# Optimization experiments

Hardware: AMD Instinct MI355X
Metric: run time of the kernel (lower is better)

The kernel has to match this reference:

```python
import jax, jax.numpy as jnp
import numpy as np

EMBED_DIM = 1024
CONTEXT_LEN = 2048
NUM_HEADS = 16
HEAD_DIM = EMBED_DIM // NUM_HEADS
BATCH = 2
SEQ = 2048


def setup_inputs() -> dict:
    key = jax.random.key(0)
    ks = jax.random.split(key, 6)
    s = 1.0 / np.sqrt(EMBED_DIM)
    x = jax.random.normal(ks[0], (BATCH, SEQ, EMBED_DIM), dtype=jnp.float32)
    # nn.Linear weights stored as [out, in]; we keep [in, out] for x @ W
    W_q = jax.random.uniform(ks[1], (EMBED_DIM, EMBED_DIM), jnp.float32, -s, s)
    W_k = jax.random.uniform(ks[2], (EMBED_DIM, EMBED_DIM), jnp.float32, -s, s)
    W_v = jax.random.uniform(ks[3], (EMBED_DIM, EMBED_DIM), jnp.float32, -s, s)
    W_o = jax.random.uniform(ks[4], (EMBED_DIM, EMBED_DIM), jnp.float32, -s, s)
    b_o = jax.random.uniform(ks[5], (EMBED_DIM,), jnp.float32, -s, s)
    return {"x": x, "W_q": W_q, "W_k": W_k, "W_v": W_v, "W_o": W_o, "b_o": b_o}


def reference(x, W_q, W_k, W_v, W_o, b_o):
    b, s, _ = x.shape
    # project and split heads: [b, s, e] -> [b, h, s, d]
    def heads(t):
        return t.reshape(b, s, NUM_HEADS, HEAD_DIM).transpose(0, 2, 1, 3)
    q = heads(x @ W_q)
    k = heads(x @ W_k)
    v = heads(x @ W_v)
    scores = jnp.einsum("bhqd,bhkd->bhqk", q, k)  # full seq x seq scores
    causal = jnp.triu(jnp.ones((s, s), dtype=bool), k=1)
    scores = jnp.where(causal, -jnp.inf, scores)
    attn = jax.nn.softmax(scores / np.sqrt(HEAD_DIM).astype(np.float32), axis=-1)
    ctx = jnp.einsum("bhqk,bhkd->bhqd", attn, v)
    ctx = ctx.transpose(0, 2, 1, 3).reshape(b, s, EMBED_DIM)
    return ctx @ W_o + b_o
```

## Files before the change

kernel.cpp:

```cpp
#include <hip/hip_runtime.h>

#define EMBED 1024
#define SEQL  2048
#define NHEAD 16
#define HDIM  64
#define NBATCH 2
#define MROWS 4096

typedef __attribute__((ext_vector_type(4))) float  f32x4;
typedef __attribute__((ext_vector_type(8))) __bf16 bf16x8;

__device__ __forceinline__ short f2bf(float f){
  __bf16 h = (__bf16)f;
  union { __bf16 h; short s; } u; u.h = h;
  return u.s;
}

#define GLDS(gp, lp) __builtin_amdgcn_global_load_lds( \
    (const __attribute__((address_space(1))) void*)(gp), \
    (__attribute__((address_space(3))) void*)(lp), 16, 0, 0)

__global__ __launch_bounds__(256) void prep_kernel(const float* __restrict__ x,
    const float* __restrict__ W0, const float* __restrict__ W1,
    const float* __restrict__ W2, const float* __restrict__ W3,
    short* __restrict__ Xb, short* __restrict__ WtAll){
  const int z = blockIdx.z;
  if (z < 4){
    __shared__ float T[64][65];
    const int idx = blockIdx.y*32 + blockIdx.x;
    if (idx >= 256) return;
    const float* W = (z==0)?W0:(z==1)?W1:(z==2)?W2:W3;
    short* Wt = WtAll + z*(EMBED*EMBED);
    const int bx = (idx & 15)*64;
    const int by = (idx >> 4)*64;
    const int c4 = (threadIdx.x & 15)*4;
    const int tr = threadIdx.x >> 4;
    #pragma unroll
    for (int i=0;i<4;++i){
      int r = 16*i + tr;
      float4 v = *(const float4*)(W + (by + r)*EMBED + bx + c4);
      T[c4+0][r] = v.x; T[c4+1][r] = v.y; T[c4+2][r] = v.z; T[c4+3][r] = v.w;
    }
    __syncthreads();
    #pragma unroll
    for (int i=0;i<4;++i){
      int n = 16*i + tr;
      short4 o;
      o.x = f2bf(T[n][c4+0]); o.y = f2bf(T[n][c4+1]);
      o.z = f2bf(T[n][c4+2]); o.w = f2bf(T[n][c4+3]);
      *(short4*)(Wt + (bx + n)*EMBED + by + c4) = o;
    }
  } else {
    const int blk = (z-4)*1024 + blockIdx.y*32 + blockIdx.x;
    const int i = (blk*256 + threadIdx.x)*4;
    float4 v = *(const float4*)(x + i);
    short4 o; o.x=f2bf(v.x); o.y=f2bf(v.y); o.z=f2bf(v.z); o.w=f2bf(v.w);
    *(short4*)(Xb + i) = o;
  }
}

__device__ __forceinline__ void gemm_tile_128(const short* __restrict__ A,
    const short* __restrict__ Bt, short* As, short* Bs, int m0, int n0, f32x4 acc[4][4]){
  const int tid  = threadIdx.x;
  const int lane = tid & 63;
  const int wid  = tid >> 6;
  const int wrow = (wid >> 1) * 64, wcol = (wid & 1) * 64;
  const int arow = tid >> 2, acol8 = (tid & 3) * 8;
  const int l15 = lane & 15, lg = lane >> 4;

  auto STAGE = [&](int b, int k0){
    short* as = As + b*4096;
    short* bs = Bs + b*4096;
    GLDS(A  + (m0      + arow) * 1024 + k0 + acol8, as + tid*8);
    GLDS(A  + (m0 + 64 + arow) * 1024 + k0 + acol8, as + 2048 + tid*8);
    GLDS(Bt + (n0      + arow) * 1024 + k0 + acol8, bs + tid*8);
    GLDS(Bt + (n0 + 64 + arow) * 1024 + k0 + acol8, bs + 2048 + tid*8);
  };

  auto KSTEP = [&](int b){
    const short* as = As + b*4096;
    const short* bs = Bs + b*4096;
    bf16x8 a[4], bb[4];
    #pragma unroll
    for (int i=0;i<4;++i) a[i]  = *(const bf16x8*)(as + (wrow+16*i+l15)*32 + 8*lg);
    #pragma unroll
    for (int j=0;j<4;++j) bb[j] = *(const bf16x8*)(bs + (wcol+16*j+l15)*32 + 8*lg);
    #pragma unroll
    for (int i=0;i<4;++i)
      #pragma unroll
      for (int j=0;j<4;++j)
        acc[i][j] = __builtin_amdgcn_mfma_f32_16x16x32_bf16(a[i], bb[j], acc[i][j], 0,0,0);
  };

  STAGE(0, 0); STAGE(1, 32);
  __syncthreads();
  for (int p = 0; p < 16; ++p){
    const int k0 = p*64;
    if (p + 1 < 16){ STAGE((2*p+2)&3, k0+64); STAGE((2*p+3)&3, k0+96); }
    KSTEP((2*p)&3);
    KSTEP((2*p+1)&3);
    __syncthreads();
  }
}

__device__ __forceinline__ void gemm_tile_64(const short* __restrict__ A,
    const short* __restrict__ Bt, short* As, short* Bs, int m0, int n0, f32x4 acc[2][4]){
  const int tid  = threadIdx.x;
  const int lane = tid & 63;
  const int wid  = tid >> 6;
  const int wrow = (wid >> 1) * 32, wcol = (wid & 1) * 64;
  const int arow = tid >> 2, acol8 = (tid & 3) * 8;
  const int l15 = lane & 15, lg = lane >> 4;

  auto STAGE = [&](int b, int k0){
    short* as = As + b*2048;
    short* bs = Bs + b*4096;
    GLDS(A  + (m0      + arow) * 1024 + k0 + acol8, as + tid*8);
    GLDS(Bt + (n0      + arow) * 1024 + k0 + acol8, bs + tid*8);
    GLDS(Bt + (n0 + 64 + arow) * 1024 + k0 + acol8, bs + 2048 + tid*8);
  };

  auto KSTEP = [&](int b){
    const short* as = As + b*2048;
    const short* bs = Bs + b*4096;
    bf16x8 a[2], bb[4];
    #pragma unroll
    for (int i=0;i<2;++i) a[i]  = *(const bf16x8*)(as + (wrow+16*i+l15)*32 + 8*lg);
    #pragma unroll
    for (int j=0;j<4;++j) bb[j] = *(const bf16x8*)(bs + (wcol+16*j+l15)*32 + 8*lg);
    #pragma unroll
    for (int i=0;i<2;++i)
      #pragma unroll
      for (int j=0;j<4;++j)
        acc[i][j] = __builtin_amdgcn_mfma_f32_16x16x32_bf16(a[i], bb[j], acc[i][j], 0,0,0);
  };

  STAGE(0, 0); STAGE(1, 32);
  __syncthreads();
  for (int p = 0; p < 16; ++p){
    const int k0 = p*64;
    if (p + 1 < 16){ STAGE((2*p+2)&3, k0+64); STAGE((2*p+3)&3, k0+96); }
    KSTEP((2*p)&3);
    KSTEP((2*p+1)&3);
    __syncthreads();
  }
}

__global__ __launch_bounds__(256) void gemm_qkv_kernel(const short* __restrict__ Xb,
    const short* __restrict__ WtAll, short* __restrict__ Q, short* __restrict__ K,
    short* __restrict__ Vt){
  __shared__ __align__(16) short SH[32768];
  short* As = SH;
  short* Bs = SH + 16384;
  const int m0 = blockIdx.x*128, n0 = blockIdx.y*128, z = blockIdx.z;
  const short* Bt = WtAll + z*(EMBED*EMBED);
  f32x4 acc[4][4] = {};
  gemm_tile_128(Xb, Bt, As, Bs, m0, n0, acc);
  const int tid  = threadIdx.x;
  const int lane = tid & 63;
  const int wid  = tid >> 6;
  const int wrow = (wid >> 1) * 64, wcol = (wid & 1) * 64;
  const int l15 = lane & 15, lg = lane >> 4;
  const int bb = m0 >> 11, srow0 = m0 & 2047;

  if (z < 2){
    short* out = z ? K : Q;
    const float qscl = (z==0) ? (0.125f * 1.44269504f) : 1.0f;
    #pragma unroll
    for (int i=0;i<4;++i)
      #pragma unroll
      for (int j=0;j<4;++j)
        #pragma unroll
        for (int r=0;r<4;++r){
          int m = m0 + wrow + 16*i + 4*lg + r;
          int n = n0 + wcol + 16*j + l15;
          int srow = m & 2047, hh = n >> 6, d = n & 63;
          out[(((bb<<4)+hh)*SEQL + srow)*HDIM + d] = f2bf(acc[i][j][r] * qscl);
        }
  } else {
    short* T = SH;
    #pragma unroll
    for (int i=0;i<4;++i)
      #pragma unroll
      for (int j=0;j<4;++j){
        int n_loc = wcol + 16*j + l15;
        int mb    = wrow + 16*i + 4*lg;
        short4 pk;
        pk.x = f2bf(acc[i][j][0]); pk.y = f2bf(acc[i][j][1]);
        pk.z = f2bf(acc[i][j][2]); pk.w = f2bf(acc[i][j][3]);
        *(short4*)(T + n_loc*128 + (mb ^ ((n_loc & 7) << 3))) = pk;
      }
    __syncthreads();
    #pragma unroll
    for (int it=0; it<8; ++it){
      int n_loc = 16*it + (tid >> 4);
      int mch   = (tid & 15) * 8;
      int4 v = *(const int4*)(T + n_loc*128 + (mch ^ ((n_loc & 7) << 3)));
      int n_glob = n0 + n_loc;
      int hh = n_glob >> 6, d = n_glob & 63;
      *(int4*)(Vt + (((bb<<4)+hh)*HDIM + d)*SEQL + srow0 + mch) = v;
    }
  }
}

__global__ __launch_bounds__(256) void gemm_out_kernel(const short* __restrict__ Ctx,
    const short* __restrict__ WtO, const float* __restrict__ bias, float* __restrict__ out){
  __shared__ __align__(16) short As[4*2048], Bs[4*4096];
  const int m0 = blockIdx.x*64, n0 = blockIdx.y*128;
  f32x4 acc[2][4] = {};
  gemm_tile_64(Ctx, WtO, As, Bs, m0, n0, acc);
  const int lane = threadIdx.x & 63;
  const int wid  = threadIdx.x >> 6;
  const int wrow = (wid >> 1) * 32, wcol = (wid & 1) * 64;
  const int l15 = lane & 15, lg = lane >> 4;
  #pragma unroll
  for (int i=0;i<2;++i)
    #pragma unroll
    for (int j=0;j<4;++j)
      #pragma unroll
      for (int r=0;r<4;++r){
        int m = m0 + wrow + 16*i + 4*lg + r;
        int n = n0 + wcol + 16*j + l15;
        out[m*EMBED + n] = acc[i][j][r] + bias[n];
      }
}

__global__ __launch_bounds__(512, 4) void attn_kernel(const short* __restrict__ Q,
    const short* __restrict__ K, const short* __restrict__ Vt, short* __restrict__ Ctx){
  __shared__ __align__(16) char lds[81920];
  const int tid  = threadIdx.x;
  const int lane = tid & 63;
  const int wid  = tid >> 6;
  const int bid   = blockIdx.x;
  const int xcd   = bid & 7;
  const int i7    = bid >> 3;
  const int bh    = xcd + 8*(i7 & 3);
  const int cidx  = i7 >> 2;
  const int chunk = (cidx < 8) ? cidx : 23 - cidx;
  const int q0blk = chunk * 128;
  const int ntp   = chunk + 1;
  const int q0w   = q0blk + 16*wid;
  const int qlast = q0w + 15;

  const short* Qh  = Q  + bh*(SEQL*HDIM);
  const char*  KhB = (const char*)(K  + bh*(SEQL*HDIM));
  const char*  VhB = (const char*)(Vt + bh*(HDIM*SEQL));
  const int l15 = lane & 15, lg = lane >> 4;
  const int lg20 = 20 * lg;
  const int swE = (l15 & 7) << 3;
  const int swB = (l15 & 7) << 4;
  const int laneRow = lane >> 3;
  const int colSwz  = 16 * ((lane & 7) ^ laneRow);
  const int r0 = 8 * wid;

  const short* qp = Qh + (q0w + l15)*HDIM + 8*lg;
  bf16x8 bq0 = *(const bf16x8*)qp;
  bf16x8 bq1 = *(const bf16x8*)(qp + 32);

  f32x4 acc[4];
  #pragma unroll
  for (int j=0; j<4; ++j) acc[j] = (f32x4){0.f,0.f,0.f,0.f};
  float mrun = -3e30f, lrun = 0.f;

  short* pw = (short*)(lds + 65536 + wid*2048);

  auto STAGE = [&](int b, int t){
    char* kb = lds + b*16384;
    char* vb = kb + 8192;
    const int kv0 = t*64;
    GLDS(KhB + (kv0 + r0 + laneRow)*128 + colSwz, kb + r0*128);
    GLDS(VhB + (r0 + laneRow)*4096 + kv0*2 + colSwz, vb + r0*128);
  };

  auto QKHALF = [&](const char* kb, f32x4 sc[4]){
    #pragma unroll
    for (int c=0; c<4; ++c){
      const char* kr = kb + (16*c + l15)*128;
      bf16x8 k0 = *(const bf16x8*)(kr + ((16*lg) ^ swB));
      bf16x8 k1 = *(const bf16x8*)(kr + ((64 + 16*lg) ^ swB));
      f32x4 zz = (f32x4){0.f,0.f,0.f,0.f};
      zz = __builtin_amdgcn_mfma_f32_16x16x32_bf16(k0, bq0, zz, 0,0,0);
      zz = __builtin_amdgcn_mfma_f32_16x16x32_bf16(k1, bq1, zz, 0,0,0);
      sc[c] = zz;
    }
  };

  STAGE(0, 0); STAGE(1, 1);
  __syncthreads();

  for (int tp = 0; tp < ntp; ++tp){
    const int t0   = 2*tp;
    const int kv00 = t0*64;
    const int kv01 = kv00 + 64;
    if (tp + 1 < ntp){ STAGE((t0+2)&3, t0+2); STAGE((t0+3)&3, t0+3); }
    if (kv00 <= qlast){
      const char* kb0 = lds + (t0&3)*16384;
      const char* kb1 = lds + ((t0+1)&3)*16384;
      const bool  h1  = (kv01 <= qlast);
      f32x4 sc0[4], sc1[4];
      __builtin_amdgcn_s_setprio(1);
      QKHALF(kb0, sc0);
      if (h1) QKHALF(kb1, sc1);
      __builtin_amdgcn_s_setprio(0);
      if (kv00 + 63 > q0w){
        #pragma unroll
        for (int c=0; c<4; ++c)
          #pragma unroll
          for (int r=0; r<4; ++r)
            if (kv00 + 16*c + 4*lg + r > q0w + l15) sc0[c][r] = -3e30f;
      }
      if (h1 && kv01 + 63 > q0w){
        #pragma unroll
        for (int c=0; c<4; ++c)
          #pragma unroll
          for (int r=0; r<4; ++r)
            if (kv01 + 16*c + 4*lg + r > q0w + l15) sc1[c][r] = -3e30f;
      }
      float cm[4];
      #pragma unroll
      for (int c=0; c<4; ++c)
        cm[c] = fmaxf(fmaxf(sc0[c][0], sc0[c][1]), fmaxf(sc0[c][2], sc0[c][3]));
      float pm = fmaxf(fmaxf(cm[0], cm[1]), fmaxf(cm[2], cm[3]));
      if (h1){
        float dm[4];
        #pragma unroll
        for (int c=0; c<4; ++c)
          dm[c] = fmaxf(fmaxf(sc1[c][0], sc1[c][1]), fmaxf(sc1[c][2], sc1[c][3]));
        pm = fmaxf(pm, fmaxf(fmaxf(dm[0], dm[1]), fmaxf(dm[2], dm[3])));
      }
      pm = fmaxf(pm, __shfl_xor(pm, 16));
      pm = fmaxf(pm, __shfl_xor(pm, 32));
      const int resc = !__all(pm <= mrun);
      float mn = mrun, ss = 1.0f;
      if (resc){
        mn = fmaxf(mrun, pm);
        ss = __builtin_amdgcn_exp2f(mrun - mn);
        mrun = mn;
      }
      #pragma unroll
      for (int c=0; c<4; ++c)
        #pragma unroll
        for (int r=0; r<4; ++r)
          sc0[c][r] = __builtin_amdgcn_exp2f(sc0[c][r] - mn);
      float cs[4];
      #pragma unroll
      for (int c=0; c<4; ++c)
        cs[c] = (sc0[c][0] + sc0[c][1]) + (sc0[c][2] + sc0[c][3]);
      float ls = (cs[0] + cs[1]) + (cs[2] + cs[3]);
      if (h1){
        #pragma unroll
        for (int c=0; c<4; ++c)
          #pragma unroll
          for (int r=0; r<4; ++r)
            sc1[c][r] = __builtin_amdgcn_exp2f(sc1[c][r] - mn);
        float ds[4];
        #pragma unroll
        for (int c=0; c<4; ++c)
          ds[c] = (sc1[c][0] + sc1[c][1]) + (sc1[c][2] + sc1[c][3]);
        ls += (ds[0] + ds[1]) + (ds[2] + ds[3]);
      }
      ls += __shfl_xor(ls, 16);
      ls += __shfl_xor(ls, 32);
      if (resc){
        lrun = lrun*ss + ls;
        float srg[4];
        #pragma unroll
        for (int r=0; r<4; ++r) srg[r] = __shfl(ss, lg20 + r);
        #pragma unroll
        for (int j=0; j<4; ++j)
          #pragma unroll
          for (int r=0; r<4; ++r) acc[j][r] *= srg[r];
      } else {
        lrun += ls;
      }
      #pragma unroll
      for (int c=0; c<4; ++c){
        short4 pk;
        pk.x = f2bf(sc0[c][0]); pk.y = f2bf(sc0[c][1]);
        pk.z = f2bf(sc0[c][2]); pk.w = f2bf(sc0[c][3]);
        *(short4*)(pw + l15*64 + ((16*c + 4*lg) ^ swE)) = pk;
      }
      {
        bf16x8 pa0 = *(const bf16x8*)(pw + l15*64 + ((8*lg)      ^ swE));
        bf16x8 pa1 = *(const bf16x8*)(pw + l15*64 + ((32 + 8*lg) ^ swE));
        const char* vb = kb0 + 8192;
        __builtin_amdgcn_s_setprio(1);
        #pragma unroll
        for (int j=0; j<4; ++j){
          const char* vrp = vb + (16*j + l15)*128;
          bf16x8 v0 = *(const bf16x8*)(vrp + ((16*lg) ^ swB));
          bf16x8 v1 = *(const bf16x8*)(vrp + ((64 + 16*lg) ^ swB));
          acc[j] = __builtin_amdgcn_mfma_f32_16x16x32_bf16(pa0, v0, acc[j], 0,0,0);
          acc[j] = __builtin_amdgcn_mfma_f32_16x16x32_bf16(pa1, v1, acc[j], 0,0,0);
        }
        __builtin_amdgcn_s_setprio(0);
      }
      if (h1){
        #pragma unroll
        for (int c=0; c<4; ++c){
          short4 pk;
          pk.x = f2bf(sc1[c][0]); pk.y = f2bf(sc1[c][1]);
          pk.z = f2bf(sc1[c][2]); pk.w = f2bf(sc1[c][3]);
          *(short4*)(pw + l15*64 + ((16*c + 4*lg) ^ swE)) = pk;
        }
        bf16x8 pa0 = *(const bf16x8*)(pw + l15*64 + ((8*lg)      ^ swE));
        bf16x8 pa1 = *(const bf16x8*)(pw + l15*64 + ((32 + 8*lg) ^ swE));
        const char* vb = kb1 + 8192;
        __builtin_amdgcn_s_setprio(1);
        #pragma unroll
        for (int j=0; j<4; ++j){
          const char* vrp = vb + (16*j + l15)*128;
          bf16x8 v0 = *(const bf16x8*)(vrp + ((16*lg) ^ swB));
          bf16x8 v1 = *(const bf16x8*)(vrp + ((64 + 16*lg) ^ swB));
          acc[j] = __builtin_amdgcn_mfma_f32_16x16x32_bf16(pa0, v0, acc[j], 0,0,0);
          acc[j] = __builtin_amdgcn_mfma_f32_16x16x32_bf16(pa1, v1, acc[j], 0,0,0);
        }
        __builtin_amdgcn_s_setprio(0);
      }
    }
    __syncthreads();
  }

  const int bb = bh >> 4, hh = bh & 15;
  float lr[4];
  #pragma unroll
  for (int r=0; r<4; ++r) lr[r] = __builtin_amdgcn_rcpf(__shfl(lrun, lg20 + r));
  #pragma unroll
  for (int j=0; j<4; ++j)
    #pragma unroll
    for (int r=0; r<4; ++r){
      int qg = q0w + 4*lg + r;
      Ctx[(bb*SEQL + qg)*EMBED + hh*HDIM + 16*j + l15] = f2bf(acc[j][r] * lr[r]);
    }
}

extern "C" void kernel_launch(void* const* d_in, const int* in_sizes, int n_in,
                              void* d_out, int out_size, void* d_ws, size_t ws_size,
                              hipStream_t stream){
  const float* x  = (const float*)d_in[0];
  const float* Wq = (const float*)d_in[1];
  const float* Wk = (const float*)d_in[2];
  const float* Wv = (const float*)d_in[3];
  const float* Wo = (const float*)d_in[4];
  const float* bo = (const float*)d_in[5];
  float* out = (float*)d_out;

  char* ws = (char*)d_ws;
  const size_t MB = 1u << 20;
  short* Xb  = (short*)(ws +  0*MB);
  short* Wt  = (short*)(ws +  8*MB);
  short* Q   = (short*)(ws + 16*MB);
  short* Kk  = (short*)(ws + 24*MB);
  short* Vt  = (short*)(ws + 32*MB);
  short* Ctx = (short*)(ws + 40*MB);

  prep_kernel<<<dim3(32,32,8), 256, 0, stream>>>(x, Wq, Wk, Wv, Wo, Xb, Wt);
  gemm_qkv_kernel<<<dim3(32,8,3), 256, 0, stream>>>(Xb, Wt, Q, Kk, Vt);
  attn_kernel<<<512, 512, 0, stream>>>(Q, Kk, Vt, Ctx);
  gemm_out_kernel<<<dim3(64,8), 256, 0, stream>>>(Ctx, Wt + 3*(EMBED*EMBED), bo, out);
}
```

Measured before the change: 101.6 us.

## Split attention KV range across wave halves with two query groups per wave

Each wave now handles 32 query rows (two 16-row groups) rather than 16, and the 8 waves are split into two halves that each process half of the causal KV tiles for the same rows. At the end, partial softmax states (max, sum, accumulator) from the second half are exchanged through LDS and merged flash-decoding style before writing the context. This is meant to balance causal work across waves and reuse each K/V fragment load for two query groups, at the cost of more registers, an extra LDS merge and a final barrier.

```diff
diff --git a/kernel.cpp b/kernel.cpp
--- a/kernel.cpp
+++ b/kernel.cpp
@@ -231,6 +231,8 @@
   const int tid  = threadIdx.x;
   const int lane = tid & 63;
   const int wid  = tid >> 6;
+  const int wrg  = wid & 3;
+  const int khalf= wid >> 2;
   const int bid   = blockIdx.x;
   const int xcd   = bid & 7;
   const int i7    = bid >> 3;
@@ -238,9 +240,12 @@
   const int cidx  = i7 >> 2;
   const int chunk = (cidx < 8) ? cidx : 23 - cidx;
   const int q0blk = chunk * 128;
-  const int ntp   = chunk + 1;
-  const int q0w   = q0blk + 16*wid;
-  const int qlast = q0w + 15;
+  const int ntblk = 2*chunk + 2;
+  const int q0w   = q0blk + 32*wrg;
+  const int nt_w  = ((q0w + 31) >> 6) + 1;
+  const int h0    = (nt_w + 1) >> 1;
+  const int tbeg  = khalf ? h0 : 0;
+  const int tend  = khalf ? nt_w : h0;
 
   const short* Qh  = Q  + bh*(SEQL*HDIM);
   const char*  KhB = (const char*)(K  + bh*(SEQL*HDIM));
@@ -253,14 +258,22 @@
   const int colSwz  = 16 * ((lane & 7) ^ laneRow);
   const int r0 = 8 * wid;
 
-  const short* qp = Qh + (q0w + l15)*HDIM + 8*lg;
-  bf16x8 bq0 = *(const bf16x8*)qp;
-  bf16x8 bq1 = *(const bf16x8*)(qp + 32);
-
-  f32x4 acc[4];
+  bf16x8 bq[2][2];
   #pragma unroll
-  for (int j=0; j<4; ++j) acc[j] = (f32x4){0.f,0.f,0.f,0.f};
-  float mrun = -3e30f, lrun = 0.f;
+  for (int g=0; g<2; ++g){
+    const short* qp = Qh + (q0w + 16*g + l15)*HDIM + 8*lg;
+    bq[g][0] = *(const bf16x8*)qp;
+    bq[g][1] = *(const bf16x8*)(qp + 32);
+  }
+
+  f32x4 acc[2][4];
+  float mrun[2], lrun[2];
+  #pragma unroll
+  for (int g=0; g<2; ++g){
+    mrun[g] = -3e30f; lrun[g] = 0.f;
+    #pragma unroll
+    for (int j=0; j<4; ++j) acc[g][j] = (f32x4){0.f,0.f,0.f,0.f};
+  }
 
   short* pw = (short*)(lds + 65536 + wid*2048);
 
@@ -272,166 +285,160 @@
     GLDS(VhB + (r0 + laneRow)*4096 + kv0*2 + colSwz, vb + r0*128);
   };
 
-  auto QKHALF = [&](const char* kb, f32x4 sc[4]){
+  auto TILE = [&](int tt){
+    const char* kb = lds + (tt&3)*16384;
+    const char* vb = kb + 8192;
+    const int kv0 = tt*64;
+    f32x4 sc[4][2];
+    __builtin_amdgcn_s_setprio(1);
     #pragma unroll
     for (int c=0; c<4; ++c){
       const char* kr = kb + (16*c + l15)*128;
       bf16x8 k0 = *(const bf16x8*)(kr + ((16*lg) ^ swB));
       bf16x8 k1 = *(const bf16x8*)(kr + ((64 + 16*lg) ^ swB));
-      f32x4 zz = (f32x4){0.f,0.f,0.f,0.f};
-      zz = __builtin_amdgcn_mfma_f32_16x16x32_bf16(k0, bq0, zz, 0,0,0);
-      zz = __builtin_amdgcn_mfma_f32_16x16x32_bf16(k1, bq1, zz, 0,0,0);
-      sc[c] = zz;
-    }
-  };
-
-  STAGE(0, 0); STAGE(1, 1);
-  __syncthreads();
-
-  for (int tp = 0; tp < ntp; ++tp){
-    const int t0   = 2*tp;
-    const int kv00 = t0*64;
-    const int kv01 = kv00 + 64;
-    if (tp + 1 < ntp){ STAGE((t0+2)&3, t0+2); STAGE((t0+3)&3, t0+3); }
-    if (kv00 <= qlast){
-      const char* kb0 = lds + (t0&3)*16384;
-      const char* kb1 = lds + ((t0+1)&3)*16384;
-      const bool  h1  = (kv01 <= qlast);
-      f32x4 sc0[4], sc1[4];
-      __builtin_amdgcn_s_setprio(1);
-      QKHALF(kb0, sc0);
-      if (h1) QKHALF(kb1, sc1);
-      __builtin_amdgcn_s_setprio(0);
-      if (kv00 + 63 > q0w){
-        #pragma unroll
-        for (int c=0; c<4; ++c)
+      #pragma unroll
+      for (int g=0; g<2; ++g){
+        f32x4 zz = (f32x4){0.f,0.f,0.f,0.f};
+        zz = __builtin_amdgcn_mfma_f32_16x16x32_bf16(k0, bq[g][0], zz, 0,0,0);
+        zz = __builtin_amdgcn_mfma_f32_16x16x32_bf16(k1, bq[g][1], zz, 0,0,0);
+        sc[c][g] = zz;
+      }
+    }
+    __builtin_amdgcn_s_setprio(0);
+    if (kv0 + 63 > q0w){
+      #pragma unroll
+      for (int c=0; c<4; ++c)
+        #pragma unroll
+        for (int g=0; g<2; ++g)
           #pragma unroll
           for (int r=0; r<4; ++r)
-            if (kv00 + 16*c + 4*lg + r > q0w + l15) sc0[c][r] = -3e30f;
-      }
-      if (h1 && kv01 + 63 > q0w){
-        #pragma unroll
-        for (int c=0; c<4; ++c)
-          #pragma unroll
-          for (int r=0; r<4; ++r)
-            if (kv01 + 16*c + 4*lg + r > q0w + l15) sc1[c][r] = -3e30f;
-      }
+            if (kv0 + 16*c + 4*lg + r > q0w + 16*g + l15) sc[c][g][r] = -3e30f;
+    }
+    #pragma unroll
+    for (int g=0; g<2; ++g){
       float cm[4];
       #pragma unroll
       for (int c=0; c<4; ++c)
-        cm[c] = fmaxf(fmaxf(sc0[c][0], sc0[c][1]), fmaxf(sc0[c][2], sc0[c][3]));
+        cm[c] = fmaxf(fmaxf(sc[c][g][0], sc[c][g][1]), fmaxf(sc[c][g][2], sc[c][g][3]));
       float pm = fmaxf(fmaxf(cm[0], cm[1]), fmaxf(cm[2], cm[3]));
-      if (h1){
-        float dm[4];
-        #pragma unroll
-        for (int c=0; c<4; ++c)
-          dm[c] = fmaxf(fmaxf(sc1[c][0], sc1[c][1]), fmaxf(sc1[c][2], sc1[c][3]));
-        pm = fmaxf(pm, fmaxf(fmaxf(dm[0], dm[1]), fmaxf(dm[2], dm[3])));
-      }
       pm = fmaxf(pm, __shfl_xor(pm, 16));
       pm = fmaxf(pm, __shfl_xor(pm, 32));
-      const int resc = !__all(pm <= mrun);
-      float mn = mrun, ss = 1.0f;
+      const int resc = !__all(pm <= mrun[g]);
+      float mn = mrun[g], ss = 1.0f;
       if (resc){
-        mn = fmaxf(mrun, pm);
-        ss = __builtin_amdgcn_exp2f(mrun - mn);
-        mrun = mn;
+        mn = fmaxf(mrun[g], pm);
+        ss = __builtin_amdgcn_exp2f(mrun[g] - mn);
+        mrun[g] = mn;
       }
       #pragma unroll
       for (int c=0; c<4; ++c)
         #pragma unroll
         for (int r=0; r<4; ++r)
-          sc0[c][r] = __builtin_amdgcn_exp2f(sc0[c][r] - mn);
+          sc[c][g][r] = __builtin_amdgcn_exp2f(sc[c][g][r] - mn);
       float cs[4];
       #pragma unroll
       for (int c=0; c<4; ++c)
-        cs[c] = (sc0[c][0] + sc0[c][1]) + (sc0[c][2] + sc0[c][3]);
+        cs[c] = (sc[c][g][0] + sc[c][g][1]) + (sc[c][g][2] + sc[c][g][3]);
       float ls = (cs[0] + cs[1]) + (cs[2] + cs[3]);
-      if (h1){
-        #pragma unroll
-        for (int c=0; c<4; ++c)
-          #pragma unroll
-          for (int r=0; r<4; ++r)
-            sc1[c][r] = __builtin_amdgcn_exp2f(sc1[c][r] - mn);
-        float ds[4];
-        #pragma unroll
-        for (int c=0; c<4; ++c)
-          ds[c] = (sc1[c][0] + sc1[c][1]) + (sc1[c][2] + sc1[c][3]);
-        ls += (ds[0] + ds[1]) + (ds[2] + ds[3]);
-      }
       ls += __shfl_xor(ls, 16);
       ls += __shfl_xor(ls, 32);
       if (resc){
-        lrun = lrun*ss + ls;
+        lrun[g] = lrun[g]*ss + ls;
         float srg[4];
         #pragma unroll
         for (int r=0; r<4; ++r) srg[r] = __shfl(ss, lg20 + r);
         #pragma unroll
         for (int j=0; j<4; ++j)
           #pragma unroll
-          for (int r=0; r<4; ++r) acc[j][r] *= srg[r];
+          for (int r=0; r<4; ++r) acc[g][j][r] *= srg[r];
       } else {
-        lrun += ls;
-      }
+        lrun[g] += ls;
+      }
+    }
+    bf16x8 pa[2][2];
+    #pragma unroll
+    for (int g=0; g<2; ++g){
       #pragma unroll
       for (int c=0; c<4; ++c){
         short4 pk;
-        pk.x = f2bf(sc0[c][0]); pk.y = f2bf(sc0[c][1]);
-        pk.z = f2bf(sc0[c][2]); pk.w = f2bf(sc0[c][3]);
+        pk.x = f2bf(sc[c][g][0]); pk.y = f2bf(sc[c][g][1]);
+        pk.z = f2bf(sc[c][g][2]); pk.w = f2bf(sc[c][g][3]);
         *(short4*)(pw + l15*64 + ((16*c + 4*lg) ^ swE)) = pk;
       }
-      {
-        bf16x8 pa0 = *(const bf16x8*)(pw + l15*64 + ((8*lg)      ^ swE));
-        bf16x8 pa1 = *(const bf16x8*)(pw + l15*64 + ((32 + 8*lg) ^ swE));
-        const char* vb = kb0 + 8192;
-        __builtin_amdgcn_s_setprio(1);
-        #pragma unroll
-        for (int j=0; j<4; ++j){
-          const char* vrp = vb + (16*j + l15)*128;
-          bf16x8 v0 = *(const bf16x8*)(vrp + ((16*lg) ^ swB));
-          bf16x8 v1 = *(const bf16x8*)(vrp + ((64 + 16*lg) ^ swB));
-          acc[j] = __builtin_amdgcn_mfma_f32_16x16x32_bf16(pa0, v0, acc[j], 0,0,0);
-          acc[j] = __builtin_amdgcn_mfma_f32_16x16x32_bf16(pa1, v1, acc[j], 0,0,0);
-        }
-        __builtin_amdgcn_s_setprio(0);
-      }
-      if (h1){
-        #pragma unroll
-        for (int c=0; c<4; ++c){
-          short4 pk;
-          pk.x = f2bf(sc1[c][0]); pk.y = f2bf(sc1[c][1]);
-          pk.z = f2bf(sc1[c][2]); pk.w = f2bf(sc1[c][3]);
-          *(short4*)(pw + l15*64 + ((16*c + 4*lg) ^ swE)) = pk;
-        }
-        bf16x8 pa0 = *(const bf16x8*)(pw + l15*64 + ((8*lg)      ^ swE));
-        bf16x8 pa1 = *(const bf16x8*)(pw + l15*64 + ((32 + 8*lg) ^ swE));
-        const char* vb = kb1 + 8192;
-        __builtin_amdgcn_s_setprio(1);
-        #pragma unroll
-        for (int j=0; j<4; ++j){
-          const char* vrp = vb + (16*j + l15)*128;
-          bf16x8 v0 = *(const bf16x8*)(vrp + ((16*lg) ^ swB));
-          bf16x8 v1 = *(const bf16x8*)(vrp + ((64 + 16*lg) ^ swB));
-          acc[j] = __builtin_amdgcn_mfma_f32_16x16x32_bf16(pa0, v0, acc[j], 0,0,0);
-          acc[j] = __builtin_amdgcn_mfma_f32_16x16x32_bf16(pa1, v1, acc[j], 0,0,0);
-        }
-        __builtin_amdgcn_s_setprio(0);
-      }
-    }
+      pa[g][0] = *(const bf16x8*)(pw + l15*64 + ((8*lg)      ^ swE));
+      pa[g][1] = *(const bf16x8*)(pw + l15*64 + ((32 + 8*lg) ^ swE));
+    }
+    __builtin_amdgcn_s_setprio(1);
+    #pragma unroll
+    for (int j=0; j<4; ++j){
+      const char* vrp = vb + (16*j + l15)*128;
+      bf16x8 v0 = *(const bf16x8*)(vrp + ((16*lg) ^ swB));
+      bf16x8 v1 = *(const bf16x8*)(vrp + ((64 + 16*lg) ^ swB));
+      #pragma unroll
+      for (int g=0; g<2; ++g){
+        acc[g][j] = __builtin_amdgcn_mfma_f32_16x16x32_bf16(pa[g][0], v0, acc[g][j], 0,0,0);
+        acc[g][j] = __builtin_amdgcn_mfma_f32_16x16x32_bf16(pa[g][1], v1, acc[g][j], 0,0,0);
+      }
+    }
+    __builtin_amdgcn_s_setprio(0);
+  };
+
+  STAGE(0, 0); STAGE(1, 1);
+  __syncthreads();
+
+  const int ntp = ntblk >> 1;
+  for (int tp = 0; tp < ntp; ++tp){
+    const int t0 = 2*tp;
+    if (tp + 1 < ntp){ STAGE((t0+2)&3, t0+2); STAGE((t0+3)&3, t0+3); }
+    if (t0   >= tbeg && t0   < tend) TILE(t0);
+    if (t0+1 >= tbeg && t0+1 < tend) TILE(t0+1);
     __syncthreads();
   }
 
+  float* Mg = (float*)lds;
+  float* Ml = (float*)(lds + 32768);
+  if (lg == 0){
+    #pragma unroll
+    for (int g=0; g<2; ++g){
+      Ml[((((wrg<<1)|khalf)<<1 | g)<<1)*16 + l15]        = mrun[g];
+      Ml[(((((wrg<<1)|khalf)<<1 | g)<<1) + 1)*16 + l15]  = lrun[g];
+    }
+  }
+  if (khalf == 1){
+    #pragma unroll
+    for (int g=0; g<2; ++g)
+      #pragma unroll
+      for (int j=0; j<4; ++j)
+        #pragma unroll
+        for (int r=0; r<4; ++r)
+          Mg[wrg*2048 + ((g*4+j)*4+r)*64 + lane] = acc[g][j][r];
+  }
+  __syncthreads();
+  if (khalf == 1) return;
+
   const int bb = bh >> 4, hh = bh & 15;
-  float lr[4];
   #pragma unroll
-  for (int r=0; r<4; ++r) lr[r] = __builtin_amdgcn_rcpf(__shfl(lrun, lg20 + r));
-  #pragma unroll
-  for (int j=0; j<4; ++j)
+  for (int g=0; g<2; ++g){
     #pragma unroll
     for (int r=0; r<4; ++r){
-      int qg = q0w + 4*lg + r;
-      Ctx[(bb*SEQL + qg)*EMBED + hh*HDIM + 16*j + l15] = f2bf(acc[j][r] * lr[r]);
-    }
+      int row = 4*lg + r;
+      float m0 = Ml[((((wrg<<1)|0)<<1 | g)<<1)*16 + row];
+      float l0 = Ml[(((((wrg<<1)|0)<<1 | g)<<1) + 1)*16 + row];
+      float m1 = Ml[((((wrg<<1)|1)<<1 | g)<<1)*16 + row];
+      float l1 = Ml[(((((wrg<<1)|1)<<1 | g)<<1) + 1)*16 + row];
+      float ms = fmaxf(m0, m1);
+      float s0 = __builtin_amdgcn_exp2f(m0 - ms);
+      float s1 = __builtin_amdgcn_exp2f(m1 - ms);
+      float rl = __builtin_amdgcn_rcpf(l0*s0 + l1*s1);
+      int qg = q0w + 16*g + row;
+      #pragma unroll
+      for (int j=0; j<4; ++j){
+        float a1 = Mg[wrg*2048 + ((g*4+j)*4+r)*64 + lane];
+        float v  = (acc[g][j][r]*s0 + a1*s1) * rl;
+        Ctx[(bb*SEQL + qg)*EMBED + hh*HDIM + 16*j + l15] = f2bf(v);
+      }
+    }
+  }
 }
 
 extern "C" void kernel_launch(void* const* d_in, const int* in_sizes, int n_in,
```

Result: slower. 115.4 us (+13.6%).
